# Kernel tuning notes

Hardware: AMD Instinct MI355X
Metric: run time of the kernel (lower is better)

The kernel has to match this reference:

```python
import jax, jax.numpy as jnp
import numpy as np

B, S, D, H = 4, 2048, 256, 8
DH = D // H
DFF = 4 * D
EPS = 1e-5


def _layernorm(x, w, b):
    mu = jnp.mean(x, axis=-1, keepdims=True)
    var = jnp.mean((x - mu) ** 2, axis=-1, keepdims=True)
    return (x - mu) * jax.lax.rsqrt(var + EPS) * w + b


def setup_inputs() -> dict:
    key = jax.random.key(0)
    ks = jax.random.split(key, 16)
    s = 0.02
    return {
        "x": jax.random.normal(ks[0], (B, S, D), jnp.float32),
        "in_proj_w": jax.random.normal(ks[1], (3 * D, D), jnp.float32) * s,
        "in_proj_b": jax.random.normal(ks[2], (3 * D,), jnp.float32) * s,
        "out_w": jax.random.normal(ks[3], (D, D), jnp.float32) * s,
        "out_b": jax.random.normal(ks[4], (D,), jnp.float32) * s,
        "ln1_w": jnp.ones((D,), jnp.float32),
        "ln1_b": jnp.zeros((D,), jnp.float32),
        "ln2_w": jnp.ones((D,), jnp.float32),
        "ln2_b": jnp.zeros((D,), jnp.float32),
        "ff1_w": jax.random.normal(ks[5], (DFF, D), jnp.float32) * s,
        "ff1_b": jax.random.normal(ks[6], (DFF,), jnp.float32) * s,
        "ff2_w": jax.random.normal(ks[7], (D, DFF), jnp.float32) * s,
        "ff2_b": jax.random.normal(ks[8], (D,), jnp.float32) * s,
        "slopes": jax.random.normal(ks[9], (H, 1, 1), jnp.float32),
    }


def reference(x, in_proj_w, in_proj_b, out_w, out_b, ln1_w, ln1_b, ln2_w, ln2_b,
              ff1_w, ff1_b, ff2_w, ff2_b, slopes):
    # learned ALiBi-style relative bias: (H, S, S)
    pos = jnp.arange(S, dtype=jnp.float32)
    rel = jnp.abs(pos[None, :] - pos[:, None])          # (S, S)
    bias = -jnp.abs(slopes) * rel[None, :, :]           # (H, S, S)

    xn = _layernorm(x, ln1_w, ln1_b)
    qkv = jnp.einsum('bsd,ed->bse', xn, in_proj_w) + in_proj_b
    q, k, v = jnp.split(qkv, 3, axis=-1)
    # (B, H, S, DH)
    q = q.reshape(B, S, H, DH).transpose(0, 2, 1, 3)
    k = k.reshape(B, S, H, DH).transpose(0, 2, 1, 3)
    v = v.reshape(B, S, H, DH).transpose(0, 2, 1, 3)

    scores = jnp.einsum('bhqd,bhkd->bhqk', q, k) / jnp.sqrt(jnp.float32(DH))
    scores = scores + bias[None, :, :, :]
    attn = jax.nn.softmax(scores, axis=-1)
    ctx = jnp.einsum('bhqk,bhkd->bhqd', attn, v)
    ctx = ctx.transpose(0, 2, 1, 3).reshape(B, S, D)
    attn_out = jnp.einsum('bsd,ed->bse', ctx, out_w) + out_b

    x = x + attn_out
    xn2 = _layernorm(x, ln2_w, ln2_b)
    h = jnp.einsum('bsd,fd->bsf', xn2, ff1_w) + ff1_b
    h = jax.nn.gelu(h, approximate=False)
    ff_out = jnp.einsum('bsf,df->bsd', h, ff2_w) + ff2_b
    return x + ff_out
```

## Files before the change

### kernel.cpp

```cpp
#include <hip/hip_runtime.h>
#include <hip/hip_bf16.h>
#include <math.h>

#define S_LEN 2048
#define D_MODEL 256
#define N_HEADS 8
#define HEAD_DIM 32
#define D_FF 1024
#define ROWS_TOTAL 8192

typedef __attribute__((ext_vector_type(8))) short short8;
typedef __attribute__((ext_vector_type(4))) float f32x4;

__device__ inline ushort f2bf(float f) {
    unsigned u = __builtin_bit_cast(unsigned, f);
    unsigned r = (u + 0x7fffu + ((u >> 16) & 1u)) >> 16;
    return (ushort)r;
}

__device__ inline float bf2f(ushort u) {
    return __builtin_bit_cast(float, ((unsigned)u) << 16);
}

__device__ inline unsigned cvtpk(float a, float b) {
    unsigned r;
    asm("v_cvt_pk_bf16_f32 %0, %1, %2" : "=v"(r) : "v"(a), "v"(b));
    return r;
}

__global__ __launch_bounds__(256) void prep_kernel(
    const float* __restrict__ w0, const float* __restrict__ w1,
    const float* __restrict__ w2, const float* __restrict__ w3,
    ushort* __restrict__ o0, ushort* __restrict__ o1,
    ushort* __restrict__ o2, ushort* __restrict__ o3,
    const float* __restrict__ x, const float* __restrict__ lnw,
    const float* __restrict__ lnb, ushort* __restrict__ xnb) {
    int blk = blockIdx.x;
    if (blk < 768) {
        int i = blk * 256 + threadIdx.x;
        const float* src;
        ushort* dst;
        int off;
        if (i < 49152)       { src = w0; dst = o0; off = i; }
        else if (i < 65536)  { src = w1; dst = o1; off = i - 49152; }
        else if (i < 131072) { src = w2; dst = o2; off = i - 65536; }
        else                 { src = w3; dst = o3; off = i - 131072; }
        float4 v = ((const float4*)src)[off];
        ushort4 u = {f2bf(v.x), f2bf(v.y), f2bf(v.z), f2bf(v.w)};
        ((ushort4*)dst)[off] = u;
    } else {
        int wid = threadIdx.x >> 6, lane = threadIdx.x & 63;
        int row = (blk - 768) * 4 + wid;
        float4 v = ((const float4*)(x + (size_t)row * D_MODEL))[lane];
        float4 wv = ((const float4*)lnw)[lane];
        float4 bv = ((const float4*)lnb)[lane];
        float s = v.x + v.y + v.z + v.w;
        float s2 = v.x * v.x + v.y * v.y + v.z * v.z + v.w * v.w;
        #pragma unroll
        for (int off2 = 1; off2 < 64; off2 <<= 1) {
            s  += __shfl_xor(s, off2);
            s2 += __shfl_xor(s2, off2);
        }
        float mu = s * (1.0f / D_MODEL);
        float var = s2 * (1.0f / D_MODEL) - mu * mu;
        float rstd = rsqrtf(var + 1e-5f);
        ushort4 o = {f2bf((v.x - mu) * rstd * wv.x + bv.x), f2bf((v.y - mu) * rstd * wv.y + bv.y),
                     f2bf((v.z - mu) * rstd * wv.z + bv.z), f2bf((v.w - mu) * rstd * wv.w + bv.w)};
        ((ushort4*)(xnb + (size_t)row * D_MODEL))[lane] = o;
    }
}

template <int EPI>
__global__ __launch_bounds__(256) void gemm_k256(
    const ushort* __restrict__ A,
    const ushort* __restrict__ W,
    const float* __restrict__ bias,
    ushort* __restrict__ outh,
    ushort* __restrict__ qout, ushort* __restrict__ kout, ushort* __restrict__ vout,
    int N) {
    __shared__ ushort As[64 * 128];
    __shared__ ushort Bs[128 * 128];
    const int tid = threadIdx.x;
    const int lane = tid & 63, wid = tid >> 6;
    const int l15 = lane & 15, hi = lane >> 4;
    const int wr = wid >> 1, wc = wid & 1;
    const int row0 = blockIdx.x * 64, col0 = blockIdx.y * 128;

    f32x4 acc[2][4];
    #pragma unroll
    for (int m = 0; m < 2; m++)
        #pragma unroll
        for (int n = 0; n < 4; n++) acc[m][n] = (f32x4){0.f, 0.f, 0.f, 0.f};

    short8 sa[4], sb[8];
    #pragma unroll
    for (int t = 0; t < 4; t++) {
        int c = tid + t * 256;
        sa[t] = *(const short8*)(A + (size_t)(row0 + (c >> 4)) * 256 + (c & 15) * 8);
    }
    #pragma unroll
    for (int t = 0; t < 8; t++) {
        int c = tid + t * 256;
        sb[t] = *(const short8*)(W + (size_t)(col0 + (c >> 4)) * 256 + (c & 15) * 8);
    }

    for (int k0 = 0; k0 < 256; k0 += 128) {
        __syncthreads();
        #pragma unroll
        for (int t = 0; t < 4; t++) {
            int c = tid + t * 256;
            int r = c >> 4, cb = (c & 15) * 16;
            *(short8*)((char*)As + r * 256 + (cb ^ ((r & 7) << 4))) = sa[t];
        }
        #pragma unroll
        for (int t = 0; t < 8; t++) {
            int c = tid + t * 256;
            int r = c >> 4, cb = (c & 15) * 16;
            *(short8*)((char*)Bs + r * 256 + (cb ^ ((r & 7) << 4))) = sb[t];
        }
        __syncthreads();
        if (k0 == 0) {
            #pragma unroll
            for (int t = 0; t < 4; t++) {
                int c = tid + t * 256;
                sa[t] = *(const short8*)(A + (size_t)(row0 + (c >> 4)) * 256 + 128 + (c & 15) * 8);
            }
            #pragma unroll
            for (int t = 0; t < 8; t++) {
                int c = tid + t * 256;
                sb[t] = *(const short8*)(W + (size_t)(col0 + (c >> 4)) * 256 + 128 + (c & 15) * 8);
            }
        }
        #pragma unroll
        for (int ks = 0; ks < 4; ks++) {
            short8 af[2], bfr[4];
            #pragma unroll
            for (int m = 0; m < 2; m++) {
                int r = wr * 32 + m * 16 + l15;
                af[m] = *(const short8*)((char*)As + r * 256 + ((ks * 64 + hi * 16) ^ ((r & 7) << 4)));
            }
            #pragma unroll
            for (int n = 0; n < 4; n++) {
                int r = wc * 64 + n * 16 + l15;
                bfr[n] = *(const short8*)((char*)Bs + r * 256 + ((ks * 64 + hi * 16) ^ ((r & 7) << 4)));
            }
            #pragma unroll
            for (int m = 0; m < 2; m++)
                #pragma unroll
                for (int n = 0; n < 4; n++)
                    acc[m][n] = __builtin_amdgcn_mfma_f32_16x16x32_bf16(af[m], bfr[n], acc[m][n], 0, 0, 0);
        }
    }

    #pragma unroll
    for (int m = 0; m < 2; m++) {
        #pragma unroll
        for (int n = 0; n < 4; n++) {
            #pragma unroll
            for (int r = 0; r < 4; r++) {
                int row = row0 + wr * 32 + m * 16 + hi * 4 + r;
                int col = col0 + wc * 64 + n * 16 + l15;
                float val = acc[m][n][r] + bias[col];
                if (EPI == 0) {
                    int part = col >> 8;
                    int d_o = col & 255;
                    int hh = d_o >> 5, dh = d_o & 31;
                    int bbb = row >> 11, s = row & 2047;
                    size_t bhi = (size_t)bbb * N_HEADS + hh;
                    if (part == 0) {
                        qout[(bhi * S_LEN + s) * HEAD_DIM + dh] = f2bf(val * 0.2550347137f);
                    } else {
                        int tt = s >> 6, k = s & 63;
                        size_t tb = (bhi * 32 + tt) * 2048;
                        if (part == 1)
                            kout[tb + (dh >> 3) * 512 + k * 8 + (dh & 7)] = f2bf(val);
                        else
                            vout[tb + ((size_t)((k >> 5) * 4 + ((k >> 3) & 3))) * 256 + dh * 8 + (k & 7)] = f2bf(val);
                    }
                } else {
                    float g = 0.5f * val * (1.f + erff(val * 0.70710678118654752f));
                    outh[(size_t)row * N + col] = f2bf(g);
                }
            }
        }
    }
}

__global__ __launch_bounds__(256) void gemm_ff2k(
    const ushort* __restrict__ A,
    const ushort* __restrict__ W,
    const float* __restrict__ bias,
    const ushort* __restrict__ resid,
    float* __restrict__ outf) {
    __shared__ ushort As[64 * 128];
    __shared__ ushort Bs[64 * 128];
    const int tid = threadIdx.x;
    const int lane = tid & 63, wid = tid >> 6;
    const int l15 = lane & 15, hi = lane >> 4;
    const int wr = wid >> 1, wc = wid & 1;
    const int row0 = blockIdx.x * 64, col0 = blockIdx.y * 64;

    f32x4 acc[2][2];
    #pragma unroll
    for (int m = 0; m < 2; m++)
        #pragma unroll
        for (int n = 0; n < 2; n++) acc[m][n] = (f32x4){0.f, 0.f, 0.f, 0.f};

    short8 sa[4], sb[4];
    #pragma unroll
    for (int t = 0; t < 4; t++) {
        int c = tid + t * 256;
        int r = c >> 4, e = (c & 15) * 8;
        sa[t] = *(const short8*)(A + (size_t)(row0 + r) * 1024 + e);
        sb[t] = *(const short8*)(W + (size_t)(col0 + r) * 1024 + e);
    }

    for (int k0 = 0; k0 < 1024; k0 += 128) {
        __syncthreads();
        #pragma unroll
        for (int t = 0; t < 4; t++) {
            int c = tid + t * 256;
            int r = c >> 4, cb = (c & 15) * 16;
            int sw = cb ^ ((r & 7) << 4);
            *(short8*)((char*)As + r * 256 + sw) = sa[t];
            *(short8*)((char*)Bs + r * 256 + sw) = sb[t];
        }
        __syncthreads();
        if (k0 + 128 < 1024) {
            #pragma unroll
            for (int t = 0; t < 4; t++) {
                int c = tid + t * 256;
                int r = c >> 4, e = (c & 15) * 8;
                sa[t] = *(const short8*)(A + (size_t)(row0 + r) * 1024 + k0 + 128 + e);
                sb[t] = *(const short8*)(W + (size_t)(col0 + r) * 1024 + k0 + 128 + e);
            }
        }
        #pragma unroll
        for (int ks = 0; ks < 4; ks++) {
            short8 af[2], bfr[2];
            #pragma unroll
            for (int m = 0; m < 2; m++) {
                int r = wr * 32 + m * 16 + l15;
                af[m] = *(const short8*)((char*)As + r * 256 + ((ks * 64 + hi * 16) ^ ((r & 7) << 4)));
            }
            #pragma unroll
            for (int n = 0; n < 2; n++) {
                int r = wc * 32 + n * 16 + l15;
                bfr[n] = *(const short8*)((char*)Bs + r * 256 + ((ks * 64 + hi * 16) ^ ((r & 7) << 4)));
            }
            #pragma unroll
            for (int m = 0; m < 2; m++)
                #pragma unroll
                for (int n = 0; n < 2; n++)
                    acc[m][n] = __builtin_amdgcn_mfma_f32_16x16x32_bf16(af[m], bfr[n], acc[m][n], 0, 0, 0);
        }
    }

    #pragma unroll
    for (int m = 0; m < 2; m++) {
        #pragma unroll
        for (int n = 0; n < 2; n++) {
            #pragma unroll
            for (int r = 0; r < 4; r++) {
                int row = row0 + wr * 32 + m * 16 + hi * 4 + r;
                int col = col0 + wc * 32 + n * 16 + l15;
                float rv = bf2f(resid[(size_t)row * 256 + col]);
                outf[(size_t)row * 256 + col] = acc[m][n][r] + bias[col] + rv;
            }
        }
    }
}

__global__ __launch_bounds__(256) void gemm_opln(
    const ushort* __restrict__ A,
    const ushort* __restrict__ W,
    const float* __restrict__ bias,
    const float* __restrict__ residf,
    const float* __restrict__ lnw, const float* __restrict__ lnb,
    ushort* __restrict__ xnb, ushort* __restrict__ x1b) {
    __shared__ ushort As[16 * 64];
    __shared__ ushort Bs[256 * 64];
    __shared__ float red[4][16][2];
    const int tid = threadIdx.x;
    const int lane = tid & 63, wc = tid >> 6;
    const int l15 = lane & 15, hi = lane >> 4;
    const int row0 = blockIdx.x * 16;

    f32x4 acc[4];
    #pragma unroll
    for (int n = 0; n < 4; n++) acc[n] = (f32x4){0.f, 0.f, 0.f, 0.f};

    short8 sa, sb[8];
    if (tid < 128)
        sa = *(const short8*)(A + (size_t)(row0 + (tid >> 3)) * 256 + (tid & 7) * 8);
    #pragma unroll
    for (int t = 0; t < 8; t++) {
        int c = tid + t * 256;
        sb[t] = *(const short8*)(W + (size_t)(c >> 3) * 256 + (c & 7) * 8);
    }

    for (int k0 = 0; k0 < 256; k0 += 64) {
        __syncthreads();
        if (tid < 128) {
            int r = tid >> 3, cb = (tid & 7) * 16;
            *(short8*)((char*)As + r * 128 + (cb ^ ((r & 7) << 4))) = sa;
        }
        #pragma unroll
        for (int t = 0; t < 8; t++) {
            int c = tid + t * 256;
            int r = c >> 3, cb = (c & 7) * 16;
            *(short8*)((char*)Bs + r * 128 + (cb ^ ((r & 7) << 4))) = sb[t];
        }
        __syncthreads();
        if (k0 + 64 < 256) {
            if (tid < 128)
                sa = *(const short8*)(A + (size_t)(row0 + (tid >> 3)) * 256 + k0 + 64 + (tid & 7) * 8);
            #pragma unroll
            for (int t = 0; t < 8; t++) {
                int c = tid + t * 256;
                sb[t] = *(const short8*)(W + (size_t)(c >> 3) * 256 + k0 + 64 + (c & 7) * 8);
            }
        }
        #pragma unroll
        for (int ks = 0; ks < 2; ks++) {
            short8 af, bfr[4];
            {
                int r = l15;
                af = *(const short8*)((char*)As + r * 128 + ((ks * 64 + hi * 16) ^ ((r & 7) << 4)));
            }
            #pragma unroll
            for (int n = 0; n < 4; n++) {
                int r = wc * 64 + n * 16 + l15;
                bfr[n] = *(const short8*)((char*)Bs + r * 128 + ((ks * 64 + hi * 16) ^ ((r & 7) << 4)));
            }
            #pragma unroll
            for (int n = 0; n < 4; n++)
                acc[n] = __builtin_amdgcn_mfma_f32_16x16x32_bf16(af, bfr[n], acc[n], 0, 0, 0);
        }
    }

    float x1v[4][4];
    float s1[4], s2[4];
    #pragma unroll
    for (int r = 0; r < 4; r++) { s1[r] = 0.f; s2[r] = 0.f; }
    #pragma unroll
    for (int n = 0; n < 4; n++) {
        #pragma unroll
        for (int r = 0; r < 4; r++) {
            int row = row0 + hi * 4 + r;
            int col = wc * 64 + n * 16 + l15;
            float v = acc[n][r] + bias[col] + residf[(size_t)row * 256 + col];
            x1v[n][r] = v;
            s1[r] += v;
            s2[r] += v * v;
        }
    }
    #pragma unroll
    for (int r = 0; r < 4; r++) {
        #pragma unroll
        for (int off = 1; off < 16; off <<= 1) {
            s1[r] += __shfl_xor(s1[r], off);
            s2[r] += __shfl_xor(s2[r], off);
        }
    }
    if (l15 == 0) {
        #pragma unroll
        for (int r = 0; r < 4; r++) {
            red[wc][hi * 4 + r][0] = s1[r];
            red[wc][hi * 4 + r][1] = s2[r];
        }
    }
    __syncthreads();
    #pragma unroll
    for (int r = 0; r < 4; r++) {
        int rl = hi * 4 + r;
        float a1 = red[0][rl][0] + red[1][rl][0] + red[2][rl][0] + red[3][rl][0];
        float a2 = red[0][rl][1] + red[1][rl][1] + red[2][rl][1] + red[3][rl][1];
        float mu = a1 * (1.0f / 256.f);
        float var = a2 * (1.0f / 256.f) - mu * mu;
        float rstd = rsqrtf(var + 1e-5f);
        size_t row = row0 + rl;
        #pragma unroll
        for (int n = 0; n < 4; n++) {
            int col = wc * 64 + n * 16 + l15;
            float v = x1v[n][r];
            xnb[row * 256 + col] = f2bf((v - mu) * rstd * lnw[col] + lnb[col]);
            x1b[row * 256 + col] = f2bf(v);
        }
    }
}

__global__ __launch_bounds__(256) void attn_mfma(
    const ushort* __restrict__ qb, const ushort* __restrict__ kb,
    const ushort* __restrict__ vt, const float* __restrict__ slopes,
    ushort* __restrict__ ctxout) {
    __shared__ ushort plds[4][1024];
    const int tid = threadIdx.x;
    const int wid = tid >> 6, lane = tid & 63;
    const int l15 = lane & 15, hi = lane >> 4;
    const int bh = blockIdx.y, h = bh & (N_HEADS - 1), bb = bh >> 3;
    const int qt = blockIdx.x * 4 + wid;
    const int qbase = qt * 16;
    const float slope = fabsf(slopes[h]) * 1.4426950408889634f;

    const int wl = (int)fminf(2048.f, 20.f / fmaxf(slope, 1e-6f));
    const int tlo = max(0, (qbase - wl) >> 6);
    const int thi = min(31, (qbase + 15 + wl) >> 6);

    const ushort* Kg = kb + (size_t)bh * 32 * 2048;
    const ushort* Vg = vt + (size_t)bh * 32 * 2048;

    short8 qf = *(const short8*)(qb + ((size_t)bh * S_LEN + qbase + l15) * HEAD_DIM + hi * 8);

    f32x4 ctxa[2];
    ctxa[0] = (f32x4){0.f, 0.f, 0.f, 0.f};
    ctxa[1] = (f32x4){0.f, 0.f, 0.f, 0.f};
    float lsum = 0.f;

    char* pw = (char*)&plds[wid][0];
    const int bpi = lane & 0x30;
    const int wr_off = ((hi >> 1) << 8) + (l15 << 4) + ((hi & 1) << 3);
    const int rd0 = (hi << 8) + (l15 << 4);

    const float qoff = (float)(qbase + l15 - 4 * hi);

    short8 kfc[4], vfc[2][2];
    {
        const ushort* Kt = Kg + (size_t)tlo * 2048;
        const ushort* Vt = Vg + (size_t)tlo * 2048;
        #pragma unroll
        for (int c = 0; c < 4; c++)
            kfc[c] = *(const short8*)(Kt + (hi * 64 + 16 * c + l15) * 8);
        #pragma unroll
        for (int f = 0; f < 2; f++)
            #pragma unroll
            for (int dt = 0; dt < 2; dt++)
                vfc[f][dt] = *(const short8*)(Vt + ((f * 4 + hi) * 32 + dt * 16 + l15) * 8);
    }

    for (int t = tlo; t <= thi; ++t) {
        short8 kfn[4], vfn[2][2];
        if (t < thi) {
            const ushort* Kt = Kg + (size_t)(t + 1) * 2048;
            const ushort* Vt = Vg + (size_t)(t + 1) * 2048;
            #pragma unroll
            for (int c = 0; c < 4; c++)
                kfn[c] = *(const short8*)(Kt + (hi * 64 + 16 * c + l15) * 8);
            #pragma unroll
            for (int f = 0; f < 2; f++)
                #pragma unroll
                for (int dt = 0; dt < 2; dt++)
                    vfn[f][dt] = *(const short8*)(Vt + ((f * 4 + hi) * 32 + dt * 16 + l15) * 8);
        }

        const f32x4 z = {0.f, 0.f, 0.f, 0.f};
        f32x4 s[4];
        __builtin_amdgcn_s_setprio(1);
        #pragma unroll
        for (int c = 0; c < 4; c++)
            s[c] = __builtin_amdgcn_mfma_f32_16x16x32_bf16(kfc[c], qf, z, 0, 0, 0);
        __builtin_amdgcn_s_setprio(0);

        float dkt = qoff - (float)(64 * t);
        #pragma unroll
        for (int c = 0; c < 4; c++) {
            float d0 = dkt - (float)(16 * c);
            #pragma unroll
            for (int r = 0; r < 4; r++)
                s[c][r] = exp2f(fmaf(-slope, fabsf(d0 - (float)r), s[c][r]));
        }
        f32x4 t01 = s[0] + s[1], t23 = s[2] + s[3];
        f32x4 tt = t01 + t23;
        float tsum = (tt[0] + tt[1]) + (tt[2] + tt[3]);
        tsum += __shfl_xor(tsum, 16);
        tsum += __shfl_xor(tsum, 32);
        lsum += tsum;

        #pragma unroll
        for (int c = 0; c < 4; c++) {
            unsigned lo  = cvtpk(s[c][0], s[c][1]);
            unsigned hi2 = cvtpk(s[c][2], s[c][3]);
            *(unsigned long long*)(pw + (c << 9) + wr_off) =
                ((unsigned long long)hi2 << 32) | (unsigned long long)lo;
        }
        asm volatile("s_waitcnt lgkmcnt(0)" ::: "memory");
        short8 pa0 = *(const short8*)(pw + rd0);
        short8 pa1 = *(const short8*)(pw + 1024 + rd0);
        __builtin_amdgcn_s_setprio(1);
        #pragma unroll
        for (int dt = 0; dt < 2; dt++) {
            ctxa[dt] = __builtin_amdgcn_mfma_f32_16x16x32_bf16(pa0, vfc[0][dt], ctxa[dt], 0, 0, 0);
            ctxa[dt] = __builtin_amdgcn_mfma_f32_16x16x32_bf16(pa1, vfc[1][dt], ctxa[dt], 0, 0, 0);
        }
        __builtin_amdgcn_s_setprio(0);

        #pragma unroll
        for (int c = 0; c < 4; c++) kfc[c] = kfn[c];
        #pragma unroll
        for (int f = 0; f < 2; f++)
            #pragma unroll
            for (int dt = 0; dt < 2; dt++) vfc[f][dt] = vfn[f][dt];
    }
    float inv = 1.f / lsum;
    int invi = __builtin_bit_cast(int, inv);
    #pragma unroll
    for (int r = 0; r < 4; r++) {
        float ir = __builtin_bit_cast(float, __builtin_amdgcn_ds_bpermute(bpi + 4 * r, invi));
        size_t row = (size_t)bb * S_LEN + qbase + 4 * hi + r;
        #pragma unroll
        for (int dt = 0; dt < 2; dt++)
            ctxout[row * D_MODEL + h * HEAD_DIM + dt * 16 + l15] = f2bf(ctxa[dt][r] * ir);
    }
}

extern "C" void kernel_launch(void* const* d_in, const int* in_sizes, int n_in,
                              void* d_out, int out_size, void* d_ws, size_t ws_size,
                              hipStream_t stream) {
    const float* x      = (const float*)d_in[0];
    const float* in_w   = (const float*)d_in[1];
    const float* in_b   = (const float*)d_in[2];
    const float* outw   = (const float*)d_in[3];
    const float* outb   = (const float*)d_in[4];
    const float* ln1w   = (const float*)d_in[5];
    const float* ln1b   = (const float*)d_in[6];
    const float* ln2w   = (const float*)d_in[7];
    const float* ln2b   = (const float*)d_in[8];
    const float* ff1w   = (const float*)d_in[9];
    const float* ff1b   = (const float*)d_in[10];
    const float* ff2w   = (const float*)d_in[11];
    const float* ff2b   = (const float*)d_in[12];
    const float* slopes = (const float*)d_in[13];
    float* out = (float*)d_out;

    const size_t SZ = (size_t)ROWS_TOTAL * D_MODEL;
    ushort* xnb   = (ushort*)d_ws;
    ushort* ctxb  = xnb + SZ;
    ushort* qb16  = ctxb + SZ;
    ushort* kb16  = qb16 + SZ;
    ushort* vt16  = kb16 + SZ;
    ushort* hbb   = vt16 + SZ;
    ushort* wqkvb = hbb + 4 * SZ;
    ushort* woutb = wqkvb + 768 * 256;
    ushort* wff1b = woutb + 256 * 256;
    ushort* wff2b = wff1b + 1024 * 256;
    ushort* x1b   = wff2b + 256 * 1024;

    prep_kernel<<<768 + ROWS_TOTAL / 4, 256, 0, stream>>>(
        in_w, outw, ff1w, ff2w, wqkvb, woutb, wff1b, wff2b, x, ln1w, ln1b, xnb);
    gemm_k256<0><<<dim3(ROWS_TOTAL / 64, 768 / 128), 256, 0, stream>>>(
        xnb, wqkvb, in_b, nullptr, qb16, kb16, vt16, 768);
    attn_mfma<<<dim3(32, 32), 256, 0, stream>>>(qb16, kb16, vt16, slopes, ctxb);
    gemm_opln<<<ROWS_TOTAL / 16, 256, 0, stream>>>(
        ctxb, woutb, outb, x, ln2w, ln2b, xnb, x1b);
    gemm_k256<2><<<dim3(ROWS_TOTAL / 64, D_FF / 128), 256, 0, stream>>>(
        xnb, wff1b, ff1b, hbb, nullptr, nullptr, nullptr, 1024);
    gemm_ff2k<<<dim3(ROWS_TOTAL / 64, D_MODEL / 64), 256, 0, stream>>>(
        hbb, wff2b, ff2b, x1b, out);
}
```

Before: 69.84 us.

## Process two 16-row query tiles per wave in ALiBi attention to reuse K/V

After: 71.06 us. About the same (+1.7%).

```diff
diff --git a/kernel.cpp b/kernel.cpp
--- a/kernel.cpp
+++ b/kernel.cpp
@@ -394,35 +394,40 @@
     const ushort* __restrict__ qb, const ushort* __restrict__ kb,
     const ushort* __restrict__ vt, const float* __restrict__ slopes,
     ushort* __restrict__ ctxout) {
-    __shared__ ushort plds[4][1024];
+    __shared__ ushort plds[4][2048];
     const int tid = threadIdx.x;
     const int wid = tid >> 6, lane = tid & 63;
     const int l15 = lane & 15, hi = lane >> 4;
     const int bh = blockIdx.y, h = bh & (N_HEADS - 1), bb = bh >> 3;
-    const int qt = blockIdx.x * 4 + wid;
-    const int qbase = qt * 16;
+    const int qbase = (blockIdx.x * 4 + wid) * 32;
     const float slope = fabsf(slopes[h]) * 1.4426950408889634f;
 
     const int wl = (int)fminf(2048.f, 20.f / fmaxf(slope, 1e-6f));
     const int tlo = max(0, (qbase - wl) >> 6);
-    const int thi = min(31, (qbase + 15 + wl) >> 6);
+    const int thi = min(31, (qbase + 31 + wl) >> 6);
 
     const ushort* Kg = kb + (size_t)bh * 32 * 2048;
     const ushort* Vg = vt + (size_t)bh * 32 * 2048;
 
-    short8 qf = *(const short8*)(qb + ((size_t)bh * S_LEN + qbase + l15) * HEAD_DIM + hi * 8);
-
-    f32x4 ctxa[2];
-    ctxa[0] = (f32x4){0.f, 0.f, 0.f, 0.f};
-    ctxa[1] = (f32x4){0.f, 0.f, 0.f, 0.f};
-    float lsum = 0.f;
+    short8 qf[2];
+    #pragma unroll
+    for (int e = 0; e < 2; e++)
+        qf[e] = *(const short8*)(qb + ((size_t)bh * S_LEN + qbase + e * 16 + l15) * HEAD_DIM + hi * 8);
+
+    f32x4 ctxa[2][2];
+    #pragma unroll
+    for (int e = 0; e < 2; e++) {
+        ctxa[e][0] = (f32x4){0.f, 0.f, 0.f, 0.f};
+        ctxa[e][1] = (f32x4){0.f, 0.f, 0.f, 0.f};
+    }
+    float lsum[2] = {0.f, 0.f};
 
     char* pw = (char*)&plds[wid][0];
     const int bpi = lane & 0x30;
     const int wr_off = ((hi >> 1) << 8) + (l15 << 4) + ((hi & 1) << 3);
     const int rd0 = (hi << 8) + (l15 << 4);
 
-    const float qoff = (float)(qbase + l15 - 4 * hi);
+    const float qoff0 = (float)(qbase + l15 - 4 * hi);
 
     short8 kfc[4], vfc[2][2];
     {
@@ -454,44 +459,54 @@
         }
 
         const f32x4 z = {0.f, 0.f, 0.f, 0.f};
-        f32x4 s[4];
+        f32x4 s[2][4];
         __builtin_amdgcn_s_setprio(1);
         #pragma unroll
-        for (int c = 0; c < 4; c++)
-            s[c] = __builtin_amdgcn_mfma_f32_16x16x32_bf16(kfc[c], qf, z, 0, 0, 0);
+        for (int e = 0; e < 2; e++)
+            #pragma unroll
+            for (int c = 0; c < 4; c++)
+                s[e][c] = __builtin_amdgcn_mfma_f32_16x16x32_bf16(kfc[c], qf[e], z, 0, 0, 0);
         __builtin_amdgcn_s_setprio(0);
 
-        float dkt = qoff - (float)(64 * t);
-        #pragma unroll
-        for (int c = 0; c < 4; c++) {
-            float d0 = dkt - (float)(16 * c);
-            #pragma unroll
-            for (int r = 0; r < 4; r++)
-                s[c][r] = exp2f(fmaf(-slope, fabsf(d0 - (float)r), s[c][r]));
-        }
-        f32x4 t01 = s[0] + s[1], t23 = s[2] + s[3];
-        f32x4 tt = t01 + t23;
-        float tsum = (tt[0] + tt[1]) + (tt[2] + tt[3]);
-        tsum += __shfl_xor(tsum, 16);
-        tsum += __shfl_xor(tsum, 32);
-        lsum += tsum;
-
-        #pragma unroll
-        for (int c = 0; c < 4; c++) {
-            unsigned lo  = cvtpk(s[c][0], s[c][1]);
-            unsigned hi2 = cvtpk(s[c][2], s[c][3]);
-            *(unsigned long long*)(pw + (c << 9) + wr_off) =
-                ((unsigned long long)hi2 << 32) | (unsigned long long)lo;
+        #pragma unroll
+        for (int e = 0; e < 2; e++) {
+            float dkt = qoff0 + (float)(16 * e) - (float)(64 * t);
+            #pragma unroll
+            for (int c = 0; c < 4; c++) {
+                float d0 = dkt - (float)(16 * c);
+                #pragma unroll
+                for (int r = 0; r < 4; r++)
+                    s[e][c][r] = exp2f(fmaf(-slope, fabsf(d0 - (float)r), s[e][c][r]));
+            }
+            f32x4 t01 = s[e][0] + s[e][1], t23 = s[e][2] + s[e][3];
+            f32x4 tt = t01 + t23;
+            float tsum = (tt[0] + tt[1]) + (tt[2] + tt[3]);
+            tsum += __shfl_xor(tsum, 16);
+            tsum += __shfl_xor(tsum, 32);
+            lsum[e] += tsum;
+            #pragma unroll
+            for (int c = 0; c < 4; c++) {
+                unsigned lo  = cvtpk(s[e][c][0], s[e][c][1]);
+                unsigned hi2 = cvtpk(s[e][c][2], s[e][c][3]);
+                *(unsigned long long*)(pw + e * 2048 + (c << 9) + wr_off) =
+                    ((unsigned long long)hi2 << 32) | (unsigned long long)lo;
+            }
         }
         asm volatile("s_waitcnt lgkmcnt(0)" ::: "memory");
-        short8 pa0 = *(const short8*)(pw + rd0);
-        short8 pa1 = *(const short8*)(pw + 1024 + rd0);
+        short8 pa[2][2];
+        #pragma unroll
+        for (int e = 0; e < 2; e++) {
+            pa[e][0] = *(const short8*)(pw + e * 2048 + rd0);
+            pa[e][1] = *(const short8*)(pw + e * 2048 + 1024 + rd0);
+        }
         __builtin_amdgcn_s_setprio(1);
         #pragma unroll
-        for (int dt = 0; dt < 2; dt++) {
-            ctxa[dt] = __builtin_amdgcn_mfma_f32_16x16x32_bf16(pa0, vfc[0][dt], ctxa[dt], 0, 0, 0);
-            ctxa[dt] = __builtin_amdgcn_mfma_f32_16x16x32_bf16(pa1, vfc[1][dt], ctxa[dt], 0, 0, 0);
-        }
+        for (int e = 0; e < 2; e++)
+            #pragma unroll
+            for (int dt = 0; dt < 2; dt++) {
+                ctxa[e][dt] = __builtin_amdgcn_mfma_f32_16x16x32_bf16(pa[e][0], vfc[0][dt], ctxa[e][dt], 0, 0, 0);
+                ctxa[e][dt] = __builtin_amdgcn_mfma_f32_16x16x32_bf16(pa[e][1], vfc[1][dt], ctxa[e][dt], 0, 0, 0);
+            }
         __builtin_amdgcn_s_setprio(0);
 
         #pragma unroll
@@ -501,15 +516,18 @@
             #pragma unroll
             for (int dt = 0; dt < 2; dt++) vfc[f][dt] = vfn[f][dt];
     }
-    float inv = 1.f / lsum;
-    int invi = __builtin_bit_cast(int, inv);
-    #pragma unroll
-    for (int r = 0; r < 4; r++) {
-        float ir = __builtin_bit_cast(float, __builtin_amdgcn_ds_bpermute(bpi + 4 * r, invi));
-        size_t row = (size_t)bb * S_LEN + qbase + 4 * hi + r;
-        #pragma unroll
-        for (int dt = 0; dt < 2; dt++)
-            ctxout[row * D_MODEL + h * HEAD_DIM + dt * 16 + l15] = f2bf(ctxa[dt][r] * ir);
+    #pragma unroll
+    for (int e = 0; e < 2; e++) {
+        float inv = 1.f / lsum[e];
+        int invi = __builtin_bit_cast(int, inv);
+        #pragma unroll
+        for (int r = 0; r < 4; r++) {
+            float ir = __builtin_bit_cast(float, __builtin_amdgcn_ds_bpermute(bpi + 4 * r, invi));
+            size_t row = (size_t)bb * S_LEN + qbase + e * 16 + 4 * hi + r;
+            #pragma unroll
+            for (int dt = 0; dt < 2; dt++)
+                ctxout[row * D_MODEL + h * HEAD_DIM + dt * 16 + l15] = f2bf(ctxa[e][dt][r] * ir);
+        }
     }
 }
 
@@ -549,7 +567,7 @@
         in_w, outw, ff1w, ff2w, wqkvb, woutb, wff1b, wff2b, x, ln1w, ln1b, xnb);
     gemm_k256<0><<<dim3(ROWS_TOTAL / 64, 768 / 128), 256, 0, stream>>>(
         xnb, wqkvb, in_b, nullptr, qb16, kb16, vt16, 768);
-    attn_mfma<<<dim3(32, 32), 256, 0, stream>>>(qb16, kb16, vt16, slopes, ctxb);
+    attn_mfma<<<dim3(16, 32), 256, 0, stream>>>(qb16, kb16, vt16, slopes, ctxb);
     gemm_opln<<<ROWS_TOTAL / 16, 256, 0, stream>>>(
         ctxb, woutb, outb, x, ln2w, ln2b, xnb, x1b);
     gemm_k256<2><<<dim3(ROWS_TOTAL / 64, D_FF / 128), 256, 0, stream>>>(
```
